# Optimization experiments

Hardware: AMD Instinct MI355X
Metric: run time of the kernel (lower is better)

Reference implementation:

```python
import jax, jax.numpy as jnp
import numpy as np

B, C, M, N = 8, 64, 256, 256
THRESHOLD = 0.8
EPS = 1e-5
PAD = 3  # kernel_size=7


def conv2d(x, w, b=None):
    # x: (B,Cin,H,W), w: (Cout,Cin,7,7), stride 1, 'same' padding 3
    y = jax.lax.conv_general_dilated(
        x, w, window_strides=(1, 1), padding=[(PAD, PAD), (PAD, PAD)],
        dimension_numbers=('NCHW', 'OIHW', 'NCHW'))
    if b is not None:
        y = y + b[None, :, None, None]
    return y


def region_norm(region, mask):
    # region: (B,C,M,N) zeroed outside region; mask: (B,C,M,N) binary
    s = jnp.sum(region, axis=(0, 2, 3))            # (C,)
    Sr = jnp.sum(mask, axis=(0, 2, 3))             # (C,)
    Sr = jnp.where(Sr == 0, 1.0, Sr)
    mu = (s / Sr)[None, :, None, None]
    t = region + (1.0 - mask) * mu                 # fill surroundings with region mean
    # BatchNorm2d(affine=False, track_running_stats=False): batch stats, biased var
    m = jnp.mean(t, axis=(0, 2, 3), keepdims=True)
    v = jnp.mean((t - m) ** 2, axis=(0, 2, 3), keepdims=True)
    bn = (t - m) * jax.lax.rsqrt(v + EPS)
    scale = jnp.sqrt(Sr / (region.shape[0] * region.shape[2] * region.shape[3]))
    return bn * scale[None, :, None, None]


def setup_inputs() -> dict:
    key = jax.random.key(0)
    k = jax.random.split(key, 6)
    x = jax.random.normal(k[0], (B, C, M, N), dtype=jnp.float32)
    # conv1: Conv2d(2,1,7,bias=False); gamma/beta: Conv2d(1,1,7) with bias
    w1 = jax.random.normal(k[1], (1, 2, 7, 7), dtype=jnp.float32) * 0.1
    wg = jax.random.normal(k[2], (1, 1, 7, 7), dtype=jnp.float32) * 0.1
    bg = jax.random.normal(k[3], (1,), dtype=jnp.float32) * 0.1
    wb = jax.random.normal(k[4], (1, 1, 7, 7), dtype=jnp.float32) * 0.1
    bb = jax.random.normal(k[5], (1,), dtype=jnp.float32) * 0.1
    return {"x": x, "w1": w1, "wg": wg, "bg": bg, "wb": wb, "bb": bb}


def reference(x, w1, wg, bg, wb, bb):
    # SelfAware_Affine
    avg_out = jnp.mean(x, axis=1, keepdims=True)       # (B,1,M,N)
    max_out = jnp.max(x, axis=1, keepdims=True)        # (B,1,M,N)
    sa_in = jnp.concatenate([avg_out, max_out], axis=1)
    sa_map = jax.nn.sigmoid(conv2d(sa_in, w1))         # (B,1,M,N)
    gamma = conv2d(sa_map, wg, bg)                     # (B,1,M,N)
    beta = conv2d(sa_map, wb, bb)                      # (B,1,M,N)
    # binary mask from detached importance map, expanded over channels
    mask = (jax.lax.stop_gradient(sa_map) >= THRESHOLD).astype(x.dtype)
    mask = jnp.broadcast_to(mask, x.shape)             # (B,C,M,N)
    rn_x = region_norm(x * mask, mask) + region_norm(x * (1.0 - mask), 1.0 - mask)
    return rn_x * (1.0 + gamma) + beta
```

## Files before the change

### kernel.cpp

```cpp
#include <hip/hip_runtime.h>
#include <cmath>

#define B_ 8
#define C_ 64
#define M_ 256
#define N_ 256
#define PLANE_ (M_*N_)
#define PIX_ (B_*PLANE_)
#define THRESH_ 0.8f
#define EPS_ 1e-5f

__global__ void k_avgmax(const float* __restrict__ x,
                         float* __restrict__ avgp, float* __restrict__ maxp) {
    int idx4 = (blockIdx.x * blockDim.x + threadIdx.x) * 4;
    int b = idx4 >> 16;
    int p = idx4 & (PLANE_ - 1);
    const float* xb = x + (size_t)b * C_ * PLANE_ + p;
    float4 s = make_float4(0.f, 0.f, 0.f, 0.f);
    float4 mx = make_float4(-INFINITY, -INFINITY, -INFINITY, -INFINITY);
    #pragma unroll 8
    for (int c = 0; c < C_; ++c) {
        float4 v = *(const float4*)(xb + (size_t)c * PLANE_);
        s.x += v.x; s.y += v.y; s.z += v.z; s.w += v.w;
        mx.x = fmaxf(mx.x, v.x); mx.y = fmaxf(mx.y, v.y);
        mx.z = fmaxf(mx.z, v.z); mx.w = fmaxf(mx.w, v.w);
    }
    const float r = 1.f / C_;
    s.x *= r; s.y *= r; s.z *= r; s.w *= r;
    *(float4*)(avgp + idx4) = s;
    *(float4*)(maxp + idx4) = mx;
}

__global__ void k_saconv(const float* __restrict__ avgp, const float* __restrict__ maxp,
                         const float* __restrict__ w1, float* __restrict__ samap) {
    __shared__ float w[98];
    if (threadIdx.x < 98) w[threadIdx.x] = w1[threadIdx.x];
    __syncthreads();
    int idx = blockIdx.x * blockDim.x + threadIdx.x;
    int b = idx >> 16;
    int r = idx & (PLANE_ - 1);
    int i = r >> 8;
    int j = r & (N_ - 1);
    const float* a = avgp + (size_t)b * PLANE_;
    const float* m = maxp + (size_t)b * PLANE_;
    float acc = 0.f;
    #pragma unroll
    for (int dh = 0; dh < 7; ++dh) {
        int ii = i + dh - 3;
        if ((unsigned)ii >= (unsigned)M_) continue;
        #pragma unroll
        for (int dw = 0; dw < 7; ++dw) {
            int jj = j + dw - 3;
            if ((unsigned)jj >= (unsigned)N_) continue;
            int o = ii * N_ + jj;
            acc += a[o] * w[dh * 7 + dw] + m[o] * w[49 + dh * 7 + dw];
        }
    }
    samap[idx] = 1.f / (1.f + expf(-acc));
}

__global__ void k_gammabeta(const float* __restrict__ samap,
                            const float* __restrict__ wg, const float* __restrict__ bgp,
                            const float* __restrict__ wb, const float* __restrict__ bbp,
                            float* __restrict__ gammap, float* __restrict__ betap,
                            unsigned char* __restrict__ maskp, int* __restrict__ cntp) {
    __shared__ float w[98];
    if (threadIdx.x < 49) w[threadIdx.x] = wg[threadIdx.x];
    else if (threadIdx.x < 98) w[threadIdx.x] = wb[threadIdx.x - 49];
    __syncthreads();
    int idx = blockIdx.x * blockDim.x + threadIdx.x;
    int b = idx >> 16;
    int r = idx & (PLANE_ - 1);
    int i = r >> 8;
    int j = r & (N_ - 1);
    const float* s = samap + (size_t)b * PLANE_;
    float g = 0.f, be = 0.f;
    #pragma unroll
    for (int dh = 0; dh < 7; ++dh) {
        int ii = i + dh - 3;
        if ((unsigned)ii >= (unsigned)M_) continue;
        #pragma unroll
        for (int dw = 0; dw < 7; ++dw) {
            int jj = j + dw - 3;
            if ((unsigned)jj >= (unsigned)N_) continue;
            float v = s[ii * N_ + jj];
            g  += v * w[dh * 7 + dw];
            be += v * w[49 + dh * 7 + dw];
        }
    }
    gammap[idx] = g + bgp[0];
    betap[idx]  = be + bbp[0];
    int mk = (samap[idx] >= THRESH_) ? 1 : 0;
    maskp[idx] = (unsigned char)mk;
    unsigned long long bal = __ballot(mk);
    __shared__ int wcnt[4];
    int wave = threadIdx.x >> 6, lane = threadIdx.x & 63;
    if (lane == 0) wcnt[wave] = __popcll(bal);
    __syncthreads();
    if (threadIdx.x == 0) {
        atomicAdd(cntp, wcnt[0] + wcnt[1] + wcnt[2] + wcnt[3]);
    }
}

__global__ void k_sums(const float* __restrict__ x, const unsigned char* __restrict__ maskp,
                       float* __restrict__ S, float* __restrict__ Q,
                       float* __restrict__ S1, float* __restrict__ Q1) {
    int chunk = blockIdx.x;
    int c = blockIdx.y;
    int b = blockIdx.z;
    const float* xp = x + ((size_t)(b * C_ + c)) * PLANE_ + chunk * 8192;
    const unsigned char* mp = maskp + (size_t)b * PLANE_ + chunk * 8192;
    float s = 0.f, q = 0.f, s1 = 0.f, q1 = 0.f;
    #pragma unroll
    for (int k = 0; k < 8; ++k) {
        int t = (k * 256 + threadIdx.x) * 4;
        float4 v = *(const float4*)(xp + t);
        uchar4 mm = *(const uchar4*)(mp + t);
        float m0 = (float)mm.x, m1 = (float)mm.y, m2 = (float)mm.z, m3 = (float)mm.w;
        s  += v.x + v.y + v.z + v.w;
        q  += v.x * v.x + v.y * v.y + v.z * v.z + v.w * v.w;
        s1 += v.x * m0 + v.y * m1 + v.z * m2 + v.w * m3;
        q1 += v.x * v.x * m0 + v.y * v.y * m1 + v.z * v.z * m2 + v.w * v.w * m3;
    }
    for (int off = 32; off > 0; off >>= 1) {
        s  += __shfl_down(s, off, 64);
        q  += __shfl_down(q, off, 64);
        s1 += __shfl_down(s1, off, 64);
        q1 += __shfl_down(q1, off, 64);
    }
    __shared__ float ls[4][4];
    int wave = threadIdx.x >> 6, lane = threadIdx.x & 63;
    if (lane == 0) { ls[wave][0] = s; ls[wave][1] = q; ls[wave][2] = s1; ls[wave][3] = q1; }
    __syncthreads();
    if (threadIdx.x == 0) {
        float ts = 0.f, tq = 0.f, ts1 = 0.f, tq1 = 0.f;
        #pragma unroll
        for (int wv = 0; wv < 4; ++wv) { ts += ls[wv][0]; tq += ls[wv][1]; ts1 += ls[wv][2]; tq1 += ls[wv][3]; }
        atomicAdd(&S[c], ts); atomicAdd(&Q[c], tq);
        atomicAdd(&S1[c], ts1); atomicAdd(&Q1[c], tq1);
    }
}

__global__ void k_coef(const float* __restrict__ S, const float* __restrict__ Q,
                       const float* __restrict__ S1, const float* __restrict__ Q1,
                       const int* __restrict__ cntp,
                       float* __restrict__ cMa, float* __restrict__ cMb,
                       float* __restrict__ cUa, float* __restrict__ cUb) {
    int c = threadIdx.x;
    if (c >= C_) return;
    const float P = (float)PIX_;
    int cnt1 = *cntp;
    float fc1 = (float)cnt1;
    float fc0 = P - fc1;
    float Sr1 = (cnt1 == 0) ? 1.f : fc1;
    float Sr0 = (cnt1 == PIX_) ? 1.f : fc0;
    float Sv = S[c], Qv = Q[c], S1v = S1[c], Q1v = Q1[c];
    float S0v = Sv - S1v, Q0v = Qv - Q1v;
    float mu1 = S1v / Sr1;
    float mu0 = S0v / Sr0;
    float m1 = (S1v + fc0 * mu1) / P;
    float v1 = fmaxf((Q1v + fc0 * mu1 * mu1) / P - m1 * m1, 0.f);
    float m0 = (S0v + fc1 * mu0) / P;
    float v0 = fmaxf((Q0v + fc1 * mu0 * mu0) / P - m0 * m0, 0.f);
    float A1 = rsqrtf(v1 + EPS_) * sqrtf(Sr1 / P);
    float A0 = rsqrtf(v0 + EPS_) * sqrtf(Sr0 / P);
    float B1 = (mu1 - m1) * A1;
    float B0 = (mu0 - m0) * A0;
    cMa[c] = A1;             cMb[c] = -m1 * A1 + B0;
    cUa[c] = A0;             cUb[c] = -m0 * A0 + B1;
}

__global__ void k_final(const float* __restrict__ x, const unsigned char* __restrict__ maskp,
                        const float* __restrict__ gammap, const float* __restrict__ betap,
                        const float* __restrict__ cMa, const float* __restrict__ cMb,
                        const float* __restrict__ cUa, const float* __restrict__ cUb,
                        float* __restrict__ out) {
    int c = blockIdx.y;
    int b = blockIdx.z;
    int p0 = blockIdx.x * 1024 + threadIdx.x * 4;
    size_t base = ((size_t)(b * C_ + c)) * PLANE_ + p0;
    int pp = b * PLANE_ + p0;
    float4 xv = *(const float4*)(x + base);
    float4 gv = *(const float4*)(gammap + pp);
    float4 bv = *(const float4*)(betap + pp);
    uchar4 mv = *(const uchar4*)(maskp + pp);
    float ma = cMa[c], mb = cMb[c], ua = cUa[c], ub = cUb[c];
    float4 o;
    o.x = (mv.x ? xv.x * ma + mb : xv.x * ua + ub) * (1.f + gv.x) + bv.x;
    o.y = (mv.y ? xv.y * ma + mb : xv.y * ua + ub) * (1.f + gv.y) + bv.y;
    o.z = (mv.z ? xv.z * ma + mb : xv.z * ua + ub) * (1.f + gv.z) + bv.z;
    o.w = (mv.w ? xv.w * ma + mb : xv.w * ua + ub) * (1.f + gv.w) + bv.w;
    *(float4*)(out + base) = o;
}

extern "C" void kernel_launch(void* const* d_in, const int* in_sizes, int n_in,
                              void* d_out, int out_size, void* d_ws, size_t ws_size,
                              hipStream_t stream) {
    const float* x  = (const float*)d_in[0];
    const float* w1 = (const float*)d_in[1];
    const float* wg = (const float*)d_in[2];
    const float* bg = (const float*)d_in[3];
    const float* wb = (const float*)d_in[4];
    const float* bb = (const float*)d_in[5];
    float* out = (float*)d_out;

    float* ws = (float*)d_ws;
    float* avgp   = ws;
    float* maxp   = avgp + PIX_;
    float* samap  = maxp + PIX_;
    float* gammap = samap + PIX_;
    float* betap  = gammap + PIX_;
    float* S   = betap + PIX_;
    float* Q   = S + C_;
    float* S1  = Q + C_;
    float* Q1  = S1 + C_;
    int*   cnt = (int*)(Q1 + C_);
    float* cMa = (float*)(cnt + 1);
    float* cMb = cMa + C_;
    float* cUa = cMb + C_;
    float* cUb = cUa + C_;
    unsigned char* maskp = (unsigned char*)(cUb + C_);

    hipMemsetAsync(S, 0, (4 * C_ + 1) * sizeof(float), stream);

    k_avgmax<<<PIX_ / (256 * 4), 256, 0, stream>>>(x, avgp, maxp);
    k_saconv<<<PIX_ / 256, 256, 0, stream>>>(avgp, maxp, w1, samap);
    k_gammabeta<<<PIX_ / 256, 256, 0, stream>>>(samap, wg, bg, wb, bb,
                                                gammap, betap, maskp, cnt);
    dim3 g3(8, C_, B_);
    k_sums<<<g3, 256, 0, stream>>>(x, maskp, S, Q, S1, Q1);
    k_coef<<<1, 64, 0, stream>>>(S, Q, S1, Q1, cnt, cMa, cMb, cUa, cUb);
    dim3 g5(PLANE_ / 1024, C_, B_);
    k_final<<<g5, 256, 0, stream>>>(x, maskp, gammap, betap, cMa, cMb, cUa, cUb, out);
}
```

Baseline: 349.4 us.

## Fuse coefficient computation into final kernel, move mask to saconv, nontemporal stores

```diff
diff --git a/kernel.cpp b/kernel.cpp
--- a/kernel.cpp
+++ b/kernel.cpp
@@ -10,6 +10,8 @@
 #define THRESH_ 0.8f
 #define EPS_ 1e-5f
 
+typedef float vfloat4 __attribute__((ext_vector_type(4)));
+
 __global__ void k_avgmax(const float* __restrict__ x,
                          float* __restrict__ avgp, float* __restrict__ maxp) {
     int idx4 = (blockIdx.x * blockDim.x + threadIdx.x) * 4;
@@ -18,7 +20,7 @@
     const float* xb = x + (size_t)b * C_ * PLANE_ + p;
     float4 s = make_float4(0.f, 0.f, 0.f, 0.f);
     float4 mx = make_float4(-INFINITY, -INFINITY, -INFINITY, -INFINITY);
-    #pragma unroll 8
+    #pragma unroll 16
     for (int c = 0; c < C_; ++c) {
         float4 v = *(const float4*)(xb + (size_t)c * PLANE_);
         s.x += v.x; s.y += v.y; s.z += v.z; s.w += v.w;
@@ -32,7 +34,8 @@
 }
 
 __global__ void k_saconv(const float* __restrict__ avgp, const float* __restrict__ maxp,
-                         const float* __restrict__ w1, float* __restrict__ samap) {
+                         const float* __restrict__ w1, float* __restrict__ samap,
+                         unsigned char* __restrict__ maskp, int* __restrict__ cntp) {
     __shared__ float w[98];
     if (threadIdx.x < 98) w[threadIdx.x] = w1[threadIdx.x];
     __syncthreads();
@@ -56,14 +59,22 @@
             acc += a[o] * w[dh * 7 + dw] + m[o] * w[49 + dh * 7 + dw];
         }
     }
-    samap[idx] = 1.f / (1.f + expf(-acc));
+    float sa = 1.f / (1.f + expf(-acc));
+    samap[idx] = sa;
+    int mk = (sa >= THRESH_) ? 1 : 0;
+    maskp[idx] = (unsigned char)mk;
+    unsigned long long bal = __ballot(mk);
+    __shared__ int wcnt[4];
+    int wave = threadIdx.x >> 6, lane = threadIdx.x & 63;
+    if (lane == 0) wcnt[wave] = __popcll(bal);
+    __syncthreads();
+    if (threadIdx.x == 0) atomicAdd(cntp, wcnt[0] + wcnt[1] + wcnt[2] + wcnt[3]);
 }
 
 __global__ void k_gammabeta(const float* __restrict__ samap,
                             const float* __restrict__ wg, const float* __restrict__ bgp,
                             const float* __restrict__ wb, const float* __restrict__ bbp,
-                            float* __restrict__ gammap, float* __restrict__ betap,
-                            unsigned char* __restrict__ maskp, int* __restrict__ cntp) {
+                            float* __restrict__ gammap, float* __restrict__ betap) {
     __shared__ float w[98];
     if (threadIdx.x < 49) w[threadIdx.x] = wg[threadIdx.x];
     else if (threadIdx.x < 98) w[threadIdx.x] = wb[threadIdx.x - 49];
@@ -90,23 +101,13 @@
     }
     gammap[idx] = g + bgp[0];
     betap[idx]  = be + bbp[0];
-    int mk = (samap[idx] >= THRESH_) ? 1 : 0;
-    maskp[idx] = (unsigned char)mk;
-    unsigned long long bal = __ballot(mk);
-    __shared__ int wcnt[4];
-    int wave = threadIdx.x >> 6, lane = threadIdx.x & 63;
-    if (lane == 0) wcnt[wave] = __popcll(bal);
-    __syncthreads();
-    if (threadIdx.x == 0) {
-        atomicAdd(cntp, wcnt[0] + wcnt[1] + wcnt[2] + wcnt[3]);
-    }
 }
 
 __global__ void k_sums(const float* __restrict__ x, const unsigned char* __restrict__ maskp,
                        float* __restrict__ S, float* __restrict__ Q,
                        float* __restrict__ S1, float* __restrict__ Q1) {
-    int chunk = blockIdx.x;
-    int c = blockIdx.y;
+    int c = blockIdx.x;
+    int chunk = blockIdx.y;
     int b = blockIdx.z;
     const float* xp = x + ((size_t)(b * C_ + c)) * PLANE_ + chunk * 8192;
     const unsigned char* mp = maskp + (size_t)b * PLANE_ + chunk * 8192;
@@ -141,13 +142,16 @@
     }
 }
 
-__global__ void k_coef(const float* __restrict__ S, const float* __restrict__ Q,
-                       const float* __restrict__ S1, const float* __restrict__ Q1,
-                       const int* __restrict__ cntp,
-                       float* __restrict__ cMa, float* __restrict__ cMb,
-                       float* __restrict__ cUa, float* __restrict__ cUb) {
-    int c = threadIdx.x;
-    if (c >= C_) return;
+__global__ void k_final(const float* __restrict__ x, const unsigned char* __restrict__ maskp,
+                        const float* __restrict__ gammap, const float* __restrict__ betap,
+                        const float* __restrict__ S, const float* __restrict__ Q,
+                        const float* __restrict__ S1, const float* __restrict__ Q1,
+                        const int* __restrict__ cntp,
+                        float* __restrict__ out) {
+    int c = blockIdx.x;
+    int b = blockIdx.z;
+    int p0 = blockIdx.y * 1024 + threadIdx.x * 4;
+
     const float P = (float)PIX_;
     int cnt1 = *cntp;
     float fc1 = (float)cnt1;
@@ -166,31 +170,21 @@
     float A0 = rsqrtf(v0 + EPS_) * sqrtf(Sr0 / P);
     float B1 = (mu1 - m1) * A1;
     float B0 = (mu0 - m0) * A0;
-    cMa[c] = A1;             cMb[c] = -m1 * A1 + B0;
-    cUa[c] = A0;             cUb[c] = -m0 * A0 + B1;
-}
-
-__global__ void k_final(const float* __restrict__ x, const unsigned char* __restrict__ maskp,
-                        const float* __restrict__ gammap, const float* __restrict__ betap,
-                        const float* __restrict__ cMa, const float* __restrict__ cMb,
-                        const float* __restrict__ cUa, const float* __restrict__ cUb,
-                        float* __restrict__ out) {
-    int c = blockIdx.y;
-    int b = blockIdx.z;
-    int p0 = blockIdx.x * 1024 + threadIdx.x * 4;
+    float ma = A1, mb = -m1 * A1 + B0;
+    float ua = A0, ub = -m0 * A0 + B1;
+
     size_t base = ((size_t)(b * C_ + c)) * PLANE_ + p0;
     int pp = b * PLANE_ + p0;
     float4 xv = *(const float4*)(x + base);
     float4 gv = *(const float4*)(gammap + pp);
     float4 bv = *(const float4*)(betap + pp);
     uchar4 mv = *(const uchar4*)(maskp + pp);
-    float ma = cMa[c], mb = cMb[c], ua = cUa[c], ub = cUb[c];
-    float4 o;
+    vfloat4 o;
     o.x = (mv.x ? xv.x * ma + mb : xv.x * ua + ub) * (1.f + gv.x) + bv.x;
     o.y = (mv.y ? xv.y * ma + mb : xv.y * ua + ub) * (1.f + gv.y) + bv.y;
     o.z = (mv.z ? xv.z * ma + mb : xv.z * ua + ub) * (1.f + gv.z) + bv.z;
     o.w = (mv.w ? xv.w * ma + mb : xv.w * ua + ub) * (1.f + gv.w) + bv.w;
-    *(float4*)(out + base) = o;
+    __builtin_nontemporal_store(o, (vfloat4*)(out + base));
 }
 
 extern "C" void kernel_launch(void* const* d_in, const int* in_sizes, int n_in,
@@ -215,21 +209,15 @@
     float* S1  = Q + C_;
     float* Q1  = S1 + C_;
     int*   cnt = (int*)(Q1 + C_);
-    float* cMa = (float*)(cnt + 1);
-    float* cMb = cMa + C_;
-    float* cUa = cMb + C_;
-    float* cUb = cUa + C_;
-    unsigned char* maskp = (unsigned char*)(cUb + C_);
-
-    hipMemsetAsync(S, 0, (4 * C_ + 1) * sizeof(float), stream);
+    unsigned char* maskp = (unsigned char*)(cnt + 1);
+
+    (void)hipMemsetAsync(S, 0, (4 * C_ + 1) * sizeof(float), stream);
 
     k_avgmax<<<PIX_ / (256 * 4), 256, 0, stream>>>(x, avgp, maxp);
-    k_saconv<<<PIX_ / 256, 256, 0, stream>>>(avgp, maxp, w1, samap);
-    k_gammabeta<<<PIX_ / 256, 256, 0, stream>>>(samap, wg, bg, wb, bb,
-                                                gammap, betap, maskp, cnt);
-    dim3 g3(8, C_, B_);
+    k_saconv<<<PIX_ / 256, 256, 0, stream>>>(avgp, maxp, w1, samap, maskp, cnt);
+    k_gammabeta<<<PIX_ / 256, 256, 0, stream>>>(samap, wg, bg, wb, bb, gammap, betap);
+    dim3 g3(C_, 8, B_);
     k_sums<<<g3, 256, 0, stream>>>(x, maskp, S, Q, S1, Q1);
-    k_coef<<<1, 64, 0, stream>>>(S, Q, S1, Q1, cnt, cMa, cMb, cUa, cUb);
-    dim3 g5(PLANE_ / 1024, C_, B_);
-    k_final<<<g5, 256, 0, stream>>>(x, maskp, gammap, betap, cMa, cMb, cUa, cUb, out);
-}
+    dim3 g5(C_, PLANE_ / 1024, B_);
+    k_final<<<g5, 256, 0, stream>>>(x, maskp, gammap, betap, S, Q, S1, Q1, cnt, out);
+}
```

Measured after the change: 350.7 us. Within noise of the previous version (+0.4%).
